# Performance work log

Measured on AMD Instinct MI355X. Metric: run time of the kernel, lower is better.

Reference implementation:

```python
import jax, jax.numpy as jnp
import numpy as np

# dims
K = 32       # num_particles
B = 32       # batch_size
T = 64       # seq_len
H = 256      # hidden_dim
E_OBS = 128  # emb_obs
E_ACT = 128  # emb_act
OBS_NUM = 64
WIN = 50     # window_length
ALPHA = 0.5  # resamp_alpha
E = E_OBS + E_ACT  # cell input size


def _lin(k, fan_in, fan_out):
    kw, kb = jax.random.split(k)
    lim = 1.0 / np.sqrt(fan_in)
    W = jax.random.uniform(kw, (fan_out, fan_in), minval=-lim, maxval=lim, dtype=jnp.float32)
    b = jax.random.uniform(kb, (fan_out,), minval=-lim, maxval=lim, dtype=jnp.float32)
    return W, b


def setup_inputs() -> dict:
    key = jax.random.key(0)
    ks = jax.random.split(key, 10)
    obs_in = jax.random.normal(ks[0], (B, T, OBS_NUM), dtype=jnp.float32)
    prev_window = jax.random.normal(ks[1], (B, T, WIN), dtype=jnp.float32)
    W_obs, b_obs = _lin(ks[2], OBS_NUM, E_OBS)
    W_act, b_act = _lin(ks[3], WIN, E_ACT)
    W_ih, b_ih = _lin(ks[4], E, 5 * H)
    W_hh, b_hh = _lin(ks[5], H, 5 * H)
    W_fcobs, b_fcobs = _lin(ks[6], H + E, 1)
    W_lab, b_lab = _lin(ks[7], H, 1)
    # init_hidden with initialize == 'rand' (torch.rand -> uniform[0,1))
    h0 = jax.random.uniform(ks[8], (K * B, H), dtype=jnp.float32)
    c0 = jax.random.uniform(ks[9], (K * B, H), dtype=jnp.float32)
    return dict(obs_in=obs_in, prev_window=prev_window, W_obs=W_obs, b_obs=b_obs,
                W_act=W_act, b_act=b_act, W_ih=W_ih, b_ih=b_ih, W_hh=W_hh, b_hh=b_hh,
                W_fcobs=W_fcobs, b_fcobs=b_fcobs, W_lab=W_lab, b_lab=b_lab, h0=h0, c0=c0)


def reference(obs_in, prev_window, W_obs, b_obs, W_act, b_act, W_ih, b_ih,
              W_hh, b_hh, W_fcobs, b_fcobs, W_lab, b_lab, h0, c0):
    # input embeddings
    obs_emb = jax.nn.relu(jnp.einsum('bto,eo->bte', obs_in, W_obs) + b_obs)
    act_emb = jax.nn.relu(jnp.einsum('btw,ew->bte', prev_window, W_act) + b_act)
    emb = jnp.concatenate([obs_emb, act_emb], axis=2)          # [B,T,E]
    emb = jnp.tile(emb, (K, 1, 1))                             # [K*B,T,E] particle-major
    xs = jnp.swapaxes(emb, 0, 1)                               # [T,K*B,E]
    p0 = jnp.full((K * B, 1), np.log(1.0 / K), dtype=jnp.float32)
    step_keys = jax.random.split(jax.random.key(42), T)        # per-step sampling keys
    offset = jnp.arange(B)

    def step(carry, inp):
        h, c, p = carry
        x, kstep = inp
        k_eps, k_res = jax.random.split(kstep)
        # PF-LSTM gates: i, f, g, o + variance head for stochastic cell state
        gates = x @ W_ih.T + b_ih + h @ W_hh.T + b_hh           # [KB,5H]
        i, f, g, o, var = jnp.split(gates, 5, axis=1)
        c1 = jax.nn.sigmoid(f) * c + jax.nn.sigmoid(i) * jnp.tanh(g)
        # reparameterization trick: c1 ~ N(c1, softplus(var)^2)
        c1 = c1 + jax.random.normal(k_eps, c1.shape, c1.dtype) * jax.nn.softplus(var)
        h1 = jax.nn.sigmoid(o) * jnp.tanh(c1)
        # observation likelihood -> particle log-weight update, normalized over particles
        logpdf = jnp.concatenate([h1, x], axis=1) @ W_fcobs.T + b_fcobs  # [KB,1]
        p1 = jax.nn.log_softmax((logpdf + p).reshape(K, B, 1), axis=0).reshape(-1, 1)
        # soft resampling: q = alpha*w + (1-alpha)/K
        rp = ALPHA * jnp.exp(p1) + (1.0 - ALPHA) / K            # [KB,1]
        logits = jnp.log(rp.reshape(K, B).T)                    # [B,K]
        idx = jax.random.categorical(k_res, logits, shape=(K, B))  # [K,B]
        flat = (offset[None, :] + idx * B).reshape(-1)          # [KB]
        h_n = h1[flat]
        c_n = c1[flat]
        # importance weight correction: w' = w / q, renormalized in log space
        pn = jnp.exp(p1.reshape(-1)[flat])
        pn = pn / (ALPHA * pn + (1.0 - ALPHA) / K)
        pn = jnp.log(pn).reshape(K, B, 1)
        pn = (pn - jax.scipy.special.logsumexp(pn, axis=0, keepdims=True)).reshape(-1, 1)
        return (h_n, c_n, pn), (h_n, pn)

    _, (hs, ps) = jax.lax.scan(step, (h0, c0, p0), (xs, step_keys))
    # hs: [T,KB,H], ps: [T,KB,1]; dropout rate is 0.0 -> identity
    w = jnp.exp(ps.reshape(T, K, B, 1))
    y = jnp.sum(hs.reshape(T, K, B, H) * w, axis=1)             # weighted particle mean [T,B,H]
    y_out = jax.nn.sigmoid(y @ W_lab.T + b_lab)                 # [T,B,1]
    pf_out = jax.nn.sigmoid(hs @ W_lab.T + b_lab)               # [T,KB,1]
    return y_out, pf_out
```

## Files before the change

### kernel.cpp

```cpp
#include <hip/hip_runtime.h>
#include <math.h>

#define KP   32
#define BB   32
#define TT   64
#define HH   256
#define KB   1024

__host__ __device__ __forceinline__ unsigned rotl32(unsigned v, int s) {
  return (v << s) | (v >> (32 - s));
}
__host__ __device__ __forceinline__ void tf2x32(unsigned k0, unsigned k1,
                                                unsigned c0, unsigned c1,
                                                unsigned& o0, unsigned& o1) {
  unsigned ks2 = k0 ^ k1 ^ 0x1BD11BDAu;
  unsigned x0 = c0 + k0, x1 = c1 + k1;
#define TF_R4(a,b,c,d)                                           \
  x0 += x1; x1 = rotl32(x1, a); x1 ^= x0;                        \
  x0 += x1; x1 = rotl32(x1, b); x1 ^= x0;                        \
  x0 += x1; x1 = rotl32(x1, c); x1 ^= x0;                        \
  x0 += x1; x1 = rotl32(x1, d); x1 ^= x0;
  TF_R4(13,15,26,6)  x0 += k1;  x1 += ks2 + 1u;
  TF_R4(17,29,16,24) x0 += ks2; x1 += k0 + 2u;
  TF_R4(13,15,26,6)  x0 += k0;  x1 += k1 + 3u;
  TF_R4(17,29,16,24) x0 += k1;  x1 += ks2 + 4u;
  TF_R4(13,15,26,6)  x0 += ks2; x1 += k0 + 5u;
#undef TF_R4
  o0 = x0; o1 = x1;
}
__device__ __forceinline__ unsigned tfx(unsigned k0, unsigned k1, unsigned ctr) {
  unsigned a, b;
  tf2x32(k0, k1, 0u, ctr, a, b);
  return a ^ b;
}

__device__ __forceinline__ float sigf(float x) { return 1.0f / (1.0f + expf(-x)); }

__device__ __forceinline__ float erfinv_f(float x) {
  float w = -log1pf(-x * x);
  float p;
  if (w < 5.0f) {
    w -= 2.5f;
    p = 2.81022636e-08f;
    p = fmaf(p, w, 3.43273939e-07f);
    p = fmaf(p, w, -3.5233877e-06f);
    p = fmaf(p, w, -4.39150654e-06f);
    p = fmaf(p, w, 0.00021858087f);
    p = fmaf(p, w, -0.00125372503f);
    p = fmaf(p, w, -0.00417768164f);
    p = fmaf(p, w, 0.246640727f);
    p = fmaf(p, w, 1.50140941f);
  } else {
    w = sqrtf(w) - 3.0f;
    p = -0.000200214257f;
    p = fmaf(p, w, 0.000100950558f);
    p = fmaf(p, w, 0.00134934322f);
    p = fmaf(p, w, -0.00367342844f);
    p = fmaf(p, w, 0.00573950773f);
    p = fmaf(p, w, -0.0076224613f);
    p = fmaf(p, w, 0.00943887047f);
    p = fmaf(p, w, 1.00167406f);
    p = fmaf(p, w, 2.83297682f);
  }
  return p * x;
}

__device__ __forceinline__ float normal_from_bits(unsigned bits) {
  float u01 = __uint_as_float(0x3f800000u | (bits >> 9)) - 1.0f;
  const float lo = -0.99999994f;
  float u = fmaxf(fmaf(u01, 2.0f, lo), lo);
  return 1.41421354f * erfinv_f(u);
}

__global__ __launch_bounds__(256) void transpose_w_kernel(
    const float* __restrict__ W, float4* __restrict__ Wt5) {
  int idx = blockIdx.x * 256 + threadIdx.x;
  int k4 = idx / 1280;
  int r  = idx - k4 * 1280;
  int h  = r / 5, g = r - h * 5;
  Wt5[idx] = *(const float4*)&W[(size_t)(g * 256 + h) * 256 + k4 * 4];
}

__global__ __launch_bounds__(256) void emb_kernel(
    const float* __restrict__ obs, const float* __restrict__ win,
    const float* __restrict__ Wobs, const float* __restrict__ bobs,
    const float* __restrict__ Wact, const float* __restrict__ bact,
    float* __restrict__ embT) {
  int r = blockIdx.x;
  int t = r >> 5, b = r & 31;
  __shared__ float xs[64];
  __shared__ float ws[50];
  int tid = threadIdx.x;
  if (tid < 64) xs[tid] = obs[(b * 64 + t) * 64 + tid];
  else if (tid < 114) ws[tid - 64] = win[(b * 64 + t) * 50 + (tid - 64)];
  __syncthreads();
  int e = tid;
  float acc = 0.0f;
  if (e < 128) {
    const float* wr = Wobs + e * 64;
    for (int o = 0; o < 64; ++o) acc = fmaf(xs[o], wr[o], acc);
    acc += bobs[e];
  } else {
    int e2 = e - 128;
    const float* wr = Wact + e2 * 50;
    for (int o = 0; o < 50; ++o) acc = fmaf(ws[o], wr[o], acc);
    acc += bact[e2];
  }
  embT[r * 256 + e] = fmaxf(acc, 0.0f);
}

__global__ __launch_bounds__(256) void xdot_kernel(
    const float* __restrict__ embT, const float* __restrict__ Wf,
    const float* __restrict__ bf, float* __restrict__ xdot) {
  int wave = threadIdx.x >> 6, lane = threadIdx.x & 63;
  int r = blockIdx.x * 4 + wave;
  const float4* row = (const float4*)(embT + (size_t)r * 256);
  const float4* wv  = (const float4*)(Wf + 256);
  float4 a = row[lane];
  float4 w = wv[lane];
  float s = a.x * w.x + a.y * w.y + a.z * w.z + a.w * w.w;
  for (int m = 1; m < 64; m <<= 1) s += __shfl_xor(s, m);
  if (lane == 0) xdot[r] = s + bf[0];
}

__global__ __launch_bounds__(256, 2) void xw_kernel(
    const float* __restrict__ embT, const float4* __restrict__ Wt5ih,
    const float* __restrict__ bih, const float* __restrict__ bhh,
    float* __restrict__ xw) {
  int cg = blockIdx.x & 7;
  int rt = blockIdx.x >> 3;
  __shared__ float h_s[64 * 256];
  int tid = threadIdx.x;
  {
    const float4* src = (const float4*)(embT + (size_t)rt * 64 * 256);
    float4* dst = (float4*)h_s;
    for (int i = tid; i < 64 * 64; i += 256) dst[i] = src[i];
  }
  __syncthreads();
  int rg = tid >> 5, hcol = tid & 31;
  int jh = cg * 32 + hcol;
  const float4* wp = Wt5ih + (size_t)jh * 5;
  const float* hb = h_s + rg * 8 * 256;
  float acc[8][5] = {};
  #pragma unroll 2
  for (int k4 = 0; k4 < 64; ++k4) {
    float4 wv[5], hv[8];
    #pragma unroll
    for (int g = 0; g < 5; ++g) wv[g] = wp[(size_t)k4 * 1280 + g];
    #pragma unroll
    for (int i = 0; i < 8; ++i)
      hv[i] = *(const float4*)&hb[i * 256 + k4 * 4];
    #pragma unroll
    for (int i = 0; i < 8; ++i)
      #pragma unroll
      for (int g = 0; g < 5; ++g) {
        acc[i][g] = fmaf(hv[i].x, wv[g].x, acc[i][g]);
        acc[i][g] = fmaf(hv[i].y, wv[g].y, acc[i][g]);
        acc[i][g] = fmaf(hv[i].z, wv[g].z, acc[i][g]);
        acc[i][g] = fmaf(hv[i].w, wv[g].w, acc[i][g]);
      }
  }
  for (int i = 0; i < 8; ++i) {
    int r = rt * 64 + rg * 8 + i;
    for (int g = 0; g < 5; ++g) {
      int j = g * 256 + jh;
      xw[(size_t)r * 1280 + j] = acc[i][g] + bih[j] + bhh[j];
    }
  }
}

__global__ __launch_bounds__(256, 2) void step_kernel(
    int t, unsigned ke0, unsigned ke1, unsigned kr0, unsigned kr1,
    const float* __restrict__ h_prev, const float* __restrict__ c_prev,
    float* __restrict__ h_next, float* __restrict__ c_next,
    const float* __restrict__ parts_prev, float* __restrict__ parts_cur,
    const float* __restrict__ labparts_prev, float* __restrict__ labparts_cur,
    const float* __restrict__ ps_prev, float* __restrict__ ps_out,
    float* __restrict__ lab_out, float* __restrict__ pf_out,
    const float* __restrict__ xdot, const float* __restrict__ xw,
    const float4* __restrict__ Wt5hh, const float* __restrict__ Wf,
    const float* __restrict__ Wlab, const float* __restrict__ blab) {
  const int tid = threadIdx.x;
  const int cg = blockIdx.x & 7;
  const int rt = blockIdx.x >> 3;

  __shared__ float sarr[1024];
  __shared__ float mtab[32], ltab[32];
  __shared__ int   flat_s[32];
  __shared__ float h_s[32 * 256];

  if (t == 0) {
    if (tid < 32) flat_s[tid] = rt * 32 + tid;
  } else {
    for (int idx = tid; idx < 1024; idx += 256) {
      float lp = 0.0f;
      #pragma unroll
      for (int c2 = 0; c2 < 8; ++c2) lp += parts_prev[c2 * 1024 + idx];
      lp += xdot[(t - 1) * 32 + (idx & 31)];
      float pp = ps_prev ? ps_prev[idx] : -3.4657359f;
      sarr[idx] = lp + pp;
    }
    __syncthreads();
    if (tid < 32) {
      const int b = tid;
      float m = -INFINITY;
      for (int k = 0; k < 32; ++k) m = fmaxf(m, sarr[k * 32 + b]);
      float s = 0.0f;
      for (int k = 0; k < 32; ++k) s += expf(sarr[k * 32 + b] - m);
      mtab[b] = m; ltab[b] = logf(s);
    }
    __syncthreads();
    {
      const int q = tid >> 3, s8 = tid & 7;
      const float m = mtab[q], l = ltab[q];
      float best = -INFINITY; int bestj = 0;
      for (int jj = 0; jj < 4; ++jj) {
        int j = s8 * 4 + jj;
        unsigned bits = tfx(kr0, kr1, (unsigned)(rt * 1024 + q * 32 + j));
        float u01 = __uint_as_float(0x3f800000u | (bits >> 9)) - 1.0f;
        float u = fmaxf(u01, 1.17549435e-38f);
        float g = -logf(-logf(u));
        float p1 = sarr[j * 32 + q] - m - l;
        float z = g + logf(fmaf(0.5f, expf(p1), 0.015625f));
        if (z > best) { best = z; bestj = j; }
      }
      #pragma unroll
      for (int mm = 1; mm < 8; mm <<= 1) {
        float ob = __shfl_xor(best, mm);
        int   oj = __shfl_xor(bestj, mm);
        if (ob > best || (ob == best && oj < bestj)) { best = ob; bestj = oj; }
      }
      if (s8 == 0) {
        int fl = bestj * 32 + q;
        flat_s[q] = fl;
        if (cg == 0) {
          float p1f = sarr[fl] - m - l;
          float e = expf(p1f);
          ps_out[rt * 32 + q] = logf(e / fmaf(0.5f, e, 0.015625f));
        }
      }
    }
    if (cg == 0) {
      __syncthreads();
      if (tid < 32) {
        int fl = flat_s[tid];
        float lab = 0.0f;
        #pragma unroll
        for (int c2 = 0; c2 < 8; ++c2) lab += labparts_prev[c2 * 1024 + fl];
        lab_out[rt * 32 + tid] = lab;
        float v = lab + blab[0];
        pf_out[rt * 32 + tid] = 1.0f / (1.0f + expf(-v));
      }
    }
  }
  __syncthreads();
  if (t >= 64) return;

  {
    float4* dst = (float4*)h_s;
    for (int i = tid; i < 32 * 64; i += 256) {
      int rr = i >> 6, kc = i & 63;
      dst[i] = *(const float4*)(h_prev + (size_t)flat_s[rr] * 256 + kc * 4);
    }
  }
  __syncthreads();

  const int rg = tid >> 5, hcol = tid & 31;
  const int jh = cg * 32 + hcol;
  const float4* wp = Wt5hh + (size_t)jh * 5;
  const float* hb = h_s + rg * 4 * 256;
  float acc[4][5] = {};
  #pragma unroll 4
  for (int k4 = 0; k4 < 64; ++k4) {
    float4 wv[5], hv[4];
    #pragma unroll
    for (int g = 0; g < 5; ++g) wv[g] = wp[(size_t)k4 * 1280 + g];
    #pragma unroll
    for (int i = 0; i < 4; ++i)
      hv[i] = *(const float4*)&hb[i * 256 + k4 * 4];
    #pragma unroll
    for (int i = 0; i < 4; ++i)
      #pragma unroll
      for (int g = 0; g < 5; ++g) {
        acc[i][g] = fmaf(hv[i].x, wv[g].x, acc[i][g]);
        acc[i][g] = fmaf(hv[i].y, wv[g].y, acc[i][g]);
        acc[i][g] = fmaf(hv[i].z, wv[g].z, acc[i][g]);
        acc[i][g] = fmaf(hv[i].w, wv[g].w, acc[i][g]);
      }
  }

  const float wfj = Wf[jh];
  const float wlj = Wlab[jh];
  #pragma unroll
  for (int i = 0; i < 4; ++i) {
    const int rl = rg * 4 + i;
    const int kb = rt * 32 + rl;
    const float* xr = xw + (size_t)(t * 32 + rl) * 1280;
    float gi = acc[i][0] + xr[jh];
    float gf = acc[i][1] + xr[256 + jh];
    float gg = acc[i][2] + xr[512 + jh];
    float go = acc[i][3] + xr[768 + jh];
    float gv = acc[i][4] + xr[1024 + jh];
    float cp = c_prev[(size_t)flat_s[rl] * 256 + jh];
    float c1 = sigf(gf) * cp + sigf(gi) * tanhf(gg);
    unsigned bits = tfx(ke0, ke1, (unsigned)(kb * 256 + jh));
    float z = normal_from_bits(bits);
    float sp = fmaxf(gv, 0.0f) + log1pf(expf(-fabsf(gv)));
    c1 = c1 + z * sp;
    float h1 = sigf(go) * tanhf(c1);
    h_next[(size_t)kb * 256 + jh] = h1;
    c_next[(size_t)kb * 256 + jh] = c1;
    float ph = h1 * wfj, pb = h1 * wlj;
    #pragma unroll
    for (int mm = 1; mm < 32; mm <<= 1) {
      ph += __shfl_xor(ph, mm);
      pb += __shfl_xor(pb, mm);
    }
    if (hcol == 0) {
      parts_cur[cg * 1024 + kb] = ph;
      labparts_cur[cg * 1024 + kb] = pb;
    }
  }
}

__global__ __launch_bounds__(256) void final_kernel(
    const float* __restrict__ ps_store, const float* __restrict__ lab_full,
    const float* __restrict__ blab, float* __restrict__ yout) {
  int idx = blockIdx.x * 256 + threadIdx.x;
  if (idx >= 2048) return;
  int t = idx >> 5, b = idx & 31;
  const float* pl = ps_store + (size_t)t * 1024 + b;
  const float* lb = lab_full + (size_t)t * 1024 + b;
  float m = -INFINITY;
  for (int k = 0; k < 32; ++k) m = fmaxf(m, pl[k * 32]);
  float num = 0.0f, den = 0.0f;
  for (int k = 0; k < 32; ++k) {
    float w = expf(pl[k * 32] - m);
    num += w * lb[k * 32];
    den += w;
  }
  float y = num / den;
  yout[idx] = 1.0f / (1.0f + expf(-(y + blab[0])));
}

extern "C" void kernel_launch(void* const* d_in, const int* in_sizes, int n_in,
                              void* d_out, int out_size, void* d_ws,
                              size_t ws_size, hipStream_t stream) {
  const float* obs  = (const float*)d_in[0];
  const float* win  = (const float*)d_in[1];
  const float* Wobs = (const float*)d_in[2];
  const float* bobs = (const float*)d_in[3];
  const float* Wact = (const float*)d_in[4];
  const float* bact = (const float*)d_in[5];
  const float* Wih  = (const float*)d_in[6];
  const float* bih  = (const float*)d_in[7];
  const float* Whh  = (const float*)d_in[8];
  const float* bhh  = (const float*)d_in[9];
  const float* Wf   = (const float*)d_in[10];
  const float* bf   = (const float*)d_in[11];
  const float* Wlab = (const float*)d_in[12];
  const float* blab = (const float*)d_in[13];
  const float* h0   = (const float*)d_in[14];
  const float* c0   = (const float*)d_in[15];
  float* out = (float*)d_out;

  char* ws = (char*)d_ws;
  float* embT = (float*)ws;                 ws += (size_t)2048 * 256 * 4;
  float* xw   = (float*)ws;                 ws += (size_t)2048 * 1280 * 4;
  float* xd   = (float*)ws;                 ws += (size_t)2048 * 4;
  float* hbuf[2]; float* cbuf[2];
  hbuf[0] = (float*)ws;                     ws += (size_t)1024 * 256 * 4;
  hbuf[1] = (float*)ws;                     ws += (size_t)1024 * 256 * 4;
  cbuf[0] = (float*)ws;                     ws += (size_t)1024 * 256 * 4;
  cbuf[1] = (float*)ws;                     ws += (size_t)1024 * 256 * 4;
  float* parts    = (float*)ws;             ws += (size_t)2 * 8 * 1024 * 4;
  float* labparts = (float*)ws;             ws += (size_t)2 * 8 * 1024 * 4;
  float* psst     = (float*)ws;             ws += (size_t)64 * 1024 * 4;
  float* labf     = (float*)ws;             ws += (size_t)64 * 1024 * 4;

  float4* Wt5ih = (float4*)hbuf[1];
  float4* Wt5hh = (float4*)embT;

  transpose_w_kernel<<<320, 256, 0, stream>>>(Wih, Wt5ih);
  emb_kernel<<<2048, 256, 0, stream>>>(obs, win, Wobs, bobs, Wact, bact, embT);
  xw_kernel<<<256, 256, 0, stream>>>(embT, Wt5ih, bih, bhh, xw);
  xdot_kernel<<<512, 256, 0, stream>>>(embT, Wf, bf, xd);
  transpose_w_kernel<<<320, 256, 0, stream>>>(Whh, Wt5hh);

  for (int t = 0; t <= 64; ++t) {
    unsigned a0, a1, ke0 = 0, ke1 = 0, kr0 = 0, kr1 = 0;
    if (t < 64) {
      tf2x32(0u, 42u, 0u, (unsigned)t, a0, a1);
      tf2x32(a0, a1, 0u, 0u, ke0, ke1);
    }
    if (t >= 1) {
      tf2x32(0u, 42u, 0u, (unsigned)(t - 1), a0, a1);
      tf2x32(a0, a1, 0u, 1u, kr0, kr1);
    }
    const float* hp = (t == 0) ? h0 : hbuf[(t - 1) & 1];
    const float* cp = (t == 0) ? c0 : cbuf[(t - 1) & 1];
    float* hn = hbuf[t & 1];
    float* cn = cbuf[t & 1];
    const float* pprev = (t >= 2) ? psst + (size_t)(t - 2) * 1024 : nullptr;
    int tm1 = (t >= 1) ? (t - 1) : 0;
    step_kernel<<<256, 256, 0, stream>>>(
        t, ke0, ke1, kr0, kr1, hp, cp, hn, cn,
        parts + (size_t)((t + 1) & 1) * 8192, parts + (size_t)(t & 1) * 8192,
        labparts + (size_t)((t + 1) & 1) * 8192,
        labparts + (size_t)(t & 1) * 8192,
        pprev, psst + (size_t)tm1 * 1024, labf + (size_t)tm1 * 1024,
        out + 2048 + (size_t)tm1 * 1024,
        xd, xw, Wt5hh, Wf, Wlab, blab);
  }

  final_kernel<<<8, 256, 0, stream>>>(psst, labf, blab, out);
  (void)in_sizes; (void)n_in; (void)out_size; (void)ws_size;
}
```

Baseline: 2.100 ms.

## Split step kernel into 32 column groups with one row per thread

The recurrent step kernel now launches 1024 blocks instead of 256. Each block covers 8 hidden columns instead of 32, and each thread computes a single row instead of four, with the particle-weight partial sums widened from 8 to 32 column groups. The shared h tile is padded to 260 floats per row to avoid LDS bank conflicts, and the launch bound asks for 4 blocks per SM. This adds parallelism and occupancy for the latency-bound recurrence, but every block now repeats the resampling prologue and gathers the full h tile. Each thread also loses register reuse of the weight loads across rows, so global weight traffic per FMA rises.

```diff
diff --git a/kernel.cpp b/kernel.cpp
--- a/kernel.cpp
+++ b/kernel.cpp
@@ -6,6 +6,7 @@
 #define TT   64
 #define HH   256
 #define KB   1024
+#define HPAD 260
 
 __host__ __device__ __forceinline__ unsigned rotl32(unsigned v, int s) {
   return (v << s) | (v >> (32 - s));
@@ -169,7 +170,7 @@
   }
 }
 
-__global__ __launch_bounds__(256, 2) void step_kernel(
+__global__ __launch_bounds__(256, 4) void step_kernel(
     int t, unsigned ke0, unsigned ke1, unsigned kr0, unsigned kr1,
     const float* __restrict__ h_prev, const float* __restrict__ c_prev,
     float* __restrict__ h_next, float* __restrict__ c_next,
@@ -181,13 +182,13 @@
     const float4* __restrict__ Wt5hh, const float* __restrict__ Wf,
     const float* __restrict__ Wlab, const float* __restrict__ blab) {
   const int tid = threadIdx.x;
-  const int cg = blockIdx.x & 7;
-  const int rt = blockIdx.x >> 3;
+  const int cg = blockIdx.x & 31;
+  const int rt = blockIdx.x >> 5;
 
   __shared__ float sarr[1024];
   __shared__ float mtab[32], ltab[32];
   __shared__ int   flat_s[32];
-  __shared__ float h_s[32 * 256];
+  __shared__ float h_s[32 * HPAD];
 
   if (t == 0) {
     if (tid < 32) flat_s[tid] = rt * 32 + tid;
@@ -195,7 +196,7 @@
     for (int idx = tid; idx < 1024; idx += 256) {
       float lp = 0.0f;
       #pragma unroll
-      for (int c2 = 0; c2 < 8; ++c2) lp += parts_prev[c2 * 1024 + idx];
+      for (int c2 = 0; c2 < 32; ++c2) lp += parts_prev[c2 * 1024 + idx];
       lp += xdot[(t - 1) * 32 + (idx & 31)];
       float pp = ps_prev ? ps_prev[idx] : -3.4657359f;
       sarr[idx] = lp + pp;
@@ -246,7 +247,7 @@
         int fl = flat_s[tid];
         float lab = 0.0f;
         #pragma unroll
-        for (int c2 = 0; c2 < 8; ++c2) lab += labparts_prev[c2 * 1024 + fl];
+        for (int c2 = 0; c2 < 32; ++c2) lab += labparts_prev[c2 * 1024 + fl];
         lab_out[rt * 32 + tid] = lab;
         float v = lab + blab[0];
         pf_out[rt * 32 + tid] = 1.0f / (1.0f + expf(-v));
@@ -256,51 +257,42 @@
   __syncthreads();
   if (t >= 64) return;
 
-  {
-    float4* dst = (float4*)h_s;
-    for (int i = tid; i < 32 * 64; i += 256) {
-      int rr = i >> 6, kc = i & 63;
-      dst[i] = *(const float4*)(h_prev + (size_t)flat_s[rr] * 256 + kc * 4);
-    }
+  for (int i = tid; i < 32 * 64; i += 256) {
+    int rr = i >> 6, kc = i & 63;
+    *(float4*)&h_s[rr * HPAD + kc * 4] =
+        *(const float4*)(h_prev + (size_t)flat_s[rr] * 256 + kc * 4);
   }
   __syncthreads();
 
-  const int rg = tid >> 5, hcol = tid & 31;
-  const int jh = cg * 32 + hcol;
+  const int rg = tid >> 3, hcol = tid & 7;
+  const int jh = cg * 8 + hcol;
   const float4* wp = Wt5hh + (size_t)jh * 5;
-  const float* hb = h_s + rg * 4 * 256;
-  float acc[4][5] = {};
+  const float* hb = h_s + rg * HPAD;
+  float acc[5] = {};
   #pragma unroll 4
   for (int k4 = 0; k4 < 64; ++k4) {
-    float4 wv[5], hv[4];
+    float4 wv[5];
     #pragma unroll
     for (int g = 0; g < 5; ++g) wv[g] = wp[(size_t)k4 * 1280 + g];
-    #pragma unroll
-    for (int i = 0; i < 4; ++i)
-      hv[i] = *(const float4*)&hb[i * 256 + k4 * 4];
-    #pragma unroll
-    for (int i = 0; i < 4; ++i)
-      #pragma unroll
-      for (int g = 0; g < 5; ++g) {
-        acc[i][g] = fmaf(hv[i].x, wv[g].x, acc[i][g]);
-        acc[i][g] = fmaf(hv[i].y, wv[g].y, acc[i][g]);
-        acc[i][g] = fmaf(hv[i].z, wv[g].z, acc[i][g]);
-        acc[i][g] = fmaf(hv[i].w, wv[g].w, acc[i][g]);
-      }
-  }
-
-  const float wfj = Wf[jh];
-  const float wlj = Wlab[jh];
-  #pragma unroll
-  for (int i = 0; i < 4; ++i) {
-    const int rl = rg * 4 + i;
+    float4 hv = *(const float4*)&hb[k4 * 4];
+    #pragma unroll
+    for (int g = 0; g < 5; ++g) {
+      acc[g] = fmaf(hv.x, wv[g].x, acc[g]);
+      acc[g] = fmaf(hv.y, wv[g].y, acc[g]);
+      acc[g] = fmaf(hv.z, wv[g].z, acc[g]);
+      acc[g] = fmaf(hv.w, wv[g].w, acc[g]);
+    }
+  }
+
+  {
+    const int rl = rg;
     const int kb = rt * 32 + rl;
     const float* xr = xw + (size_t)(t * 32 + rl) * 1280;
-    float gi = acc[i][0] + xr[jh];
-    float gf = acc[i][1] + xr[256 + jh];
-    float gg = acc[i][2] + xr[512 + jh];
-    float go = acc[i][3] + xr[768 + jh];
-    float gv = acc[i][4] + xr[1024 + jh];
+    float gi = acc[0] + xr[jh];
+    float gf = acc[1] + xr[256 + jh];
+    float gg = acc[2] + xr[512 + jh];
+    float go = acc[3] + xr[768 + jh];
+    float gv = acc[4] + xr[1024 + jh];
     float cp = c_prev[(size_t)flat_s[rl] * 256 + jh];
     float c1 = sigf(gf) * cp + sigf(gi) * tanhf(gg);
     unsigned bits = tfx(ke0, ke1, (unsigned)(kb * 256 + jh));
@@ -310,9 +302,9 @@
     float h1 = sigf(go) * tanhf(c1);
     h_next[(size_t)kb * 256 + jh] = h1;
     c_next[(size_t)kb * 256 + jh] = c1;
-    float ph = h1 * wfj, pb = h1 * wlj;
-    #pragma unroll
-    for (int mm = 1; mm < 32; mm <<= 1) {
+    float ph = h1 * Wf[jh], pb = h1 * Wlab[jh];
+    #pragma unroll
+    for (int mm = 1; mm < 8; mm <<= 1) {
       ph += __shfl_xor(ph, mm);
       pb += __shfl_xor(pb, mm);
     }
@@ -373,8 +365,8 @@
   hbuf[1] = (float*)ws;                     ws += (size_t)1024 * 256 * 4;
   cbuf[0] = (float*)ws;                     ws += (size_t)1024 * 256 * 4;
   cbuf[1] = (float*)ws;                     ws += (size_t)1024 * 256 * 4;
-  float* parts    = (float*)ws;             ws += (size_t)2 * 8 * 1024 * 4;
-  float* labparts = (float*)ws;             ws += (size_t)2 * 8 * 1024 * 4;
+  float* parts    = (float*)ws;             ws += (size_t)2 * 32 * 1024 * 4;
+  float* labparts = (float*)ws;             ws += (size_t)2 * 32 * 1024 * 4;
   float* psst     = (float*)ws;             ws += (size_t)64 * 1024 * 4;
   float* labf     = (float*)ws;             ws += (size_t)64 * 1024 * 4;
 
@@ -403,11 +395,11 @@
     float* cn = cbuf[t & 1];
     const float* pprev = (t >= 2) ? psst + (size_t)(t - 2) * 1024 : nullptr;
     int tm1 = (t >= 1) ? (t - 1) : 0;
-    step_kernel<<<256, 256, 0, stream>>>(
+    step_kernel<<<1024, 256, 0, stream>>>(
         t, ke0, ke1, kr0, kr1, hp, cp, hn, cn,
-        parts + (size_t)((t + 1) & 1) * 8192, parts + (size_t)(t & 1) * 8192,
-        labparts + (size_t)((t + 1) & 1) * 8192,
-        labparts + (size_t)(t & 1) * 8192,
+        parts + (size_t)((t + 1) & 1) * 32768, parts + (size_t)(t & 1) * 32768,
+        labparts + (size_t)((t + 1) & 1) * 32768,
+        labparts + (size_t)(t & 1) * 32768,
         pprev, psst + (size_t)tm1 * 1024, labf + (size_t)tm1 * 1024,
         out + 2048 + (size_t)tm1 * 1024,
         xd, xw, Wt5hh, Wf, Wlab, blab);
```

Measured after the change: 4.647 ms. 121% more time.

## Split step kernel over 16 column groups with padded shared h and row-major partials

Applied to the files above, without the earlier changes.

Each step launch now uses 512 blocks instead of 256, each covering 16 hidden columns and 2 rows per thread group, so more CUs work on the recurrent matvec. The hh weights are re-laid out per gate so neighbouring threads read contiguous float4s. Shared h rows are padded to cut LDS bank conflicts. Partial dot products are stored particle-major with 16 entries so the reduction reads them with vector loads. The trade-off is that every block still repeats the logsumexp and resampling prologue, now twice as many times, and each block does less arithmetic per weight load.

```diff
diff --git a/kernel.cpp b/kernel.cpp
--- a/kernel.cpp
+++ b/kernel.cpp
@@ -6,6 +6,7 @@
 #define TT   64
 #define HH   256
 #define KB   1024
+#define HPAD 264
 
 __host__ __device__ __forceinline__ unsigned rotl32(unsigned v, int s) {
   return (v << s) | (v >> (32 - s));
@@ -72,7 +73,14 @@
   return 1.41421354f * erfinv_f(u);
 }
 
-__global__ __launch_bounds__(256) void transpose_w_kernel(
+__global__ __launch_bounds__(256) void transpose_w4_kernel(
+    const float* __restrict__ W, float4* __restrict__ Wt4) {
+  int idx = blockIdx.x * 256 + threadIdx.x;
+  int k4 = idx / 1280, j = idx - k4 * 1280;
+  Wt4[idx] = *(const float4*)&W[(size_t)j * 256 + k4 * 4];
+}
+
+__global__ __launch_bounds__(256) void transpose_w5_kernel(
     const float* __restrict__ W, float4* __restrict__ Wt5) {
   int idx = blockIdx.x * 256 + threadIdx.x;
   int k4 = idx / 1280;
@@ -178,24 +186,28 @@
     const float* __restrict__ ps_prev, float* __restrict__ ps_out,
     float* __restrict__ lab_out, float* __restrict__ pf_out,
     const float* __restrict__ xdot, const float* __restrict__ xw,
-    const float4* __restrict__ Wt5hh, const float* __restrict__ Wf,
+    const float4* __restrict__ Wt4hh, const float* __restrict__ Wf,
     const float* __restrict__ Wlab, const float* __restrict__ blab) {
   const int tid = threadIdx.x;
-  const int cg = blockIdx.x & 7;
-  const int rt = blockIdx.x >> 3;
+  const int cg = blockIdx.x & 15;
+  const int rt = blockIdx.x >> 4;
 
   __shared__ float sarr[1024];
   __shared__ float mtab[32], ltab[32];
   __shared__ int   flat_s[32];
-  __shared__ float h_s[32 * 256];
+  __shared__ float h_s[32 * HPAD];
 
   if (t == 0) {
     if (tid < 32) flat_s[tid] = rt * 32 + tid;
   } else {
     for (int idx = tid; idx < 1024; idx += 256) {
+      const float4* pr = (const float4*)(parts_prev + (size_t)idx * 16);
+      float4 p0 = pr[0], p1 = pr[1], p2 = pr[2], p3 = pr[3];
       float lp = 0.0f;
-      #pragma unroll
-      for (int c2 = 0; c2 < 8; ++c2) lp += parts_prev[c2 * 1024 + idx];
+      lp += p0.x; lp += p0.y; lp += p0.z; lp += p0.w;
+      lp += p1.x; lp += p1.y; lp += p1.z; lp += p1.w;
+      lp += p2.x; lp += p2.y; lp += p2.z; lp += p2.w;
+      lp += p3.x; lp += p3.y; lp += p3.z; lp += p3.w;
       lp += xdot[(t - 1) * 32 + (idx & 31)];
       float pp = ps_prev ? ps_prev[idx] : -3.4657359f;
       sarr[idx] = lp + pp;
@@ -244,9 +256,13 @@
       __syncthreads();
       if (tid < 32) {
         int fl = flat_s[tid];
+        const float4* lpp = (const float4*)(labparts_prev + (size_t)fl * 16);
+        float4 p0 = lpp[0], p1 = lpp[1], p2 = lpp[2], p3 = lpp[3];
         float lab = 0.0f;
-        #pragma unroll
-        for (int c2 = 0; c2 < 8; ++c2) lab += labparts_prev[c2 * 1024 + fl];
+        lab += p0.x; lab += p0.y; lab += p0.z; lab += p0.w;
+        lab += p1.x; lab += p1.y; lab += p1.z; lab += p1.w;
+        lab += p2.x; lab += p2.y; lab += p2.z; lab += p2.w;
+        lab += p3.x; lab += p3.y; lab += p3.z; lab += p3.w;
         lab_out[rt * 32 + tid] = lab;
         float v = lab + blab[0];
         pf_out[rt * 32 + tid] = 1.0f / (1.0f + expf(-v));
@@ -256,44 +272,42 @@
   __syncthreads();
   if (t >= 64) return;
 
-  {
-    float4* dst = (float4*)h_s;
-    for (int i = tid; i < 32 * 64; i += 256) {
-      int rr = i >> 6, kc = i & 63;
-      dst[i] = *(const float4*)(h_prev + (size_t)flat_s[rr] * 256 + kc * 4);
-    }
+  for (int i = tid; i < 32 * 64; i += 256) {
+    int rr = i >> 6, kc = i & 63;
+    *(float4*)&h_s[rr * HPAD + kc * 4] =
+        *(const float4*)(h_prev + (size_t)flat_s[rr] * 256 + kc * 4);
   }
   __syncthreads();
 
-  const int rg = tid >> 5, hcol = tid & 31;
-  const int jh = cg * 32 + hcol;
-  const float4* wp = Wt5hh + (size_t)jh * 5;
-  const float* hb = h_s + rg * 4 * 256;
-  float acc[4][5] = {};
+  const int rg = tid >> 4, hcol = tid & 15;
+  const int jh = cg * 16 + hcol;
+  const float* hb = h_s + rg * 2 * HPAD;
+  float acc[2][5] = {};
   #pragma unroll 4
   for (int k4 = 0; k4 < 64; ++k4) {
-    float4 wv[5], hv[4];
-    #pragma unroll
-    for (int g = 0; g < 5; ++g) wv[g] = wp[(size_t)k4 * 1280 + g];
-    #pragma unroll
-    for (int i = 0; i < 4; ++i)
-      hv[i] = *(const float4*)&hb[i * 256 + k4 * 4];
-    #pragma unroll
-    for (int i = 0; i < 4; ++i)
-      #pragma unroll
-      for (int g = 0; g < 5; ++g) {
-        acc[i][g] = fmaf(hv[i].x, wv[g].x, acc[i][g]);
-        acc[i][g] = fmaf(hv[i].y, wv[g].y, acc[i][g]);
-        acc[i][g] = fmaf(hv[i].z, wv[g].z, acc[i][g]);
-        acc[i][g] = fmaf(hv[i].w, wv[g].w, acc[i][g]);
-      }
+    float4 wv[5], hv0, hv1;
+    #pragma unroll
+    for (int g = 0; g < 5; ++g) wv[g] = Wt4hh[k4 * 1280 + g * 256 + jh];
+    hv0 = *(const float4*)&hb[k4 * 4];
+    hv1 = *(const float4*)&hb[HPAD + k4 * 4];
+    #pragma unroll
+    for (int g = 0; g < 5; ++g) {
+      acc[0][g] = fmaf(hv0.x, wv[g].x, acc[0][g]);
+      acc[0][g] = fmaf(hv0.y, wv[g].y, acc[0][g]);
+      acc[0][g] = fmaf(hv0.z, wv[g].z, acc[0][g]);
+      acc[0][g] = fmaf(hv0.w, wv[g].w, acc[0][g]);
+      acc[1][g] = fmaf(hv1.x, wv[g].x, acc[1][g]);
+      acc[1][g] = fmaf(hv1.y, wv[g].y, acc[1][g]);
+      acc[1][g] = fmaf(hv1.z, wv[g].z, acc[1][g]);
+      acc[1][g] = fmaf(hv1.w, wv[g].w, acc[1][g]);
+    }
   }
 
   const float wfj = Wf[jh];
   const float wlj = Wlab[jh];
   #pragma unroll
-  for (int i = 0; i < 4; ++i) {
-    const int rl = rg * 4 + i;
+  for (int i = 0; i < 2; ++i) {
+    const int rl = rg * 2 + i;
     const int kb = rt * 32 + rl;
     const float* xr = xw + (size_t)(t * 32 + rl) * 1280;
     float gi = acc[i][0] + xr[jh];
@@ -312,13 +326,13 @@
     c_next[(size_t)kb * 256 + jh] = c1;
     float ph = h1 * wfj, pb = h1 * wlj;
     #pragma unroll
-    for (int mm = 1; mm < 32; mm <<= 1) {
+    for (int mm = 1; mm < 16; mm <<= 1) {
       ph += __shfl_xor(ph, mm);
       pb += __shfl_xor(pb, mm);
     }
     if (hcol == 0) {
-      parts_cur[cg * 1024 + kb] = ph;
-      labparts_cur[cg * 1024 + kb] = pb;
+      parts_cur[(size_t)kb * 16 + cg] = ph;
+      labparts_cur[(size_t)kb * 16 + cg] = pb;
     }
   }
 }
@@ -373,19 +387,19 @@
   hbuf[1] = (float*)ws;                     ws += (size_t)1024 * 256 * 4;
   cbuf[0] = (float*)ws;                     ws += (size_t)1024 * 256 * 4;
   cbuf[1] = (float*)ws;                     ws += (size_t)1024 * 256 * 4;
-  float* parts    = (float*)ws;             ws += (size_t)2 * 8 * 1024 * 4;
-  float* labparts = (float*)ws;             ws += (size_t)2 * 8 * 1024 * 4;
+  float* parts    = (float*)ws;             ws += (size_t)2 * 16 * 1024 * 4;
+  float* labparts = (float*)ws;             ws += (size_t)2 * 16 * 1024 * 4;
   float* psst     = (float*)ws;             ws += (size_t)64 * 1024 * 4;
   float* labf     = (float*)ws;             ws += (size_t)64 * 1024 * 4;
 
   float4* Wt5ih = (float4*)hbuf[1];
-  float4* Wt5hh = (float4*)embT;
-
-  transpose_w_kernel<<<320, 256, 0, stream>>>(Wih, Wt5ih);
+  float4* Wt4hh = (float4*)embT;
+
+  transpose_w5_kernel<<<320, 256, 0, stream>>>(Wih, Wt5ih);
   emb_kernel<<<2048, 256, 0, stream>>>(obs, win, Wobs, bobs, Wact, bact, embT);
   xw_kernel<<<256, 256, 0, stream>>>(embT, Wt5ih, bih, bhh, xw);
   xdot_kernel<<<512, 256, 0, stream>>>(embT, Wf, bf, xd);
-  transpose_w_kernel<<<320, 256, 0, stream>>>(Whh, Wt5hh);
+  transpose_w4_kernel<<<320, 256, 0, stream>>>(Whh, Wt4hh);
 
   for (int t = 0; t <= 64; ++t) {
     unsigned a0, a1, ke0 = 0, ke1 = 0, kr0 = 0, kr1 = 0;
@@ -403,14 +417,14 @@
     float* cn = cbuf[t & 1];
     const float* pprev = (t >= 2) ? psst + (size_t)(t - 2) * 1024 : nullptr;
     int tm1 = (t >= 1) ? (t - 1) : 0;
-    step_kernel<<<256, 256, 0, stream>>>(
+    step_kernel<<<512, 256, 0, stream>>>(
         t, ke0, ke1, kr0, kr1, hp, cp, hn, cn,
-        parts + (size_t)((t + 1) & 1) * 8192, parts + (size_t)(t & 1) * 8192,
-        labparts + (size_t)((t + 1) & 1) * 8192,
-        labparts + (size_t)(t & 1) * 8192,
+        parts + (size_t)((t + 1) & 1) * 16384, parts + (size_t)(t & 1) * 16384,
+        labparts + (size_t)((t + 1) & 1) * 16384,
+        labparts + (size_t)(t & 1) * 16384,
         pprev, psst + (size_t)tm1 * 1024, labf + (size_t)tm1 * 1024,
         out + 2048 + (size_t)tm1 * 1024,
-        xd, xw, Wt5hh, Wf, Wlab, blab);
+        xd, xw, Wt4hh, Wf, Wlab, blab);
   }
 
   final_kernel<<<8, 256, 0, stream>>>(psst, labf, blab, out);
```

New measurement: 2.444 ms. 16.4% more time.
